# Optimization experiments

Measured on AMD Instinct MI355X. Metric: run time of the kernel, lower is better.

## Reference

```python
import jax, jax.numpy as jnp
import numpy as np
import math

D_MODEL = 1024
NUM_HEADS = 16


def setup_inputs() -> dict:
    key = jax.random.key(0)
    ks = jax.random.split(key, 5)
    B, S, D = 4, 2048, D_MODEL
    scale = 1.0 / math.sqrt(D)
    x = jax.random.normal(ks[0], (B, S, D), dtype=jnp.float32)
    wq = jax.random.normal(ks[1], (D, D), dtype=jnp.float32) * scale
    wk = jax.random.normal(ks[2], (D, D), dtype=jnp.float32) * scale
    wv = jax.random.normal(ks[3], (D, D), dtype=jnp.float32) * scale
    wo = jax.random.normal(ks[4], (D, D), dtype=jnp.float32) * scale
    return {"x": x, "wq": wq, "wk": wk, "wv": wv, "wo": wo}


def _mhsa(x, wq, wk, wv, wo):
    B, S, D = x.shape
    H = NUM_HEADS
    dk = D // H
    # projections: y = x @ W^T
    q = (x @ wq.T).reshape(B, S, H, dk).transpose(0, 2, 1, 3)  # [B,H,S,dk]
    k = (x @ wk.T).reshape(B, S, H, dk).transpose(0, 2, 1, 3)
    v = (x @ wv.T).reshape(B, S, H, dk).transpose(0, 2, 1, 3)
    scores = jnp.einsum("bhqd,bhkd->bhqk", q, k) / jnp.sqrt(jnp.asarray(dk, x.dtype))
    mask = jnp.tril(jnp.ones((S, S), dtype=bool))  # [S,S] causal
    neg_inf = jnp.asarray(-jnp.inf, scores.dtype)
    scores_masked = jnp.where(mask, scores, neg_inf)
    max_scores = jnp.max(scores_masked, axis=-1, keepdims=True)
    max_scores = jnp.where(jnp.isfinite(max_scores), max_scores, jnp.zeros_like(max_scores))
    exp_scores = jnp.exp(scores - max_scores) * mask.astype(scores.dtype)
    denom = jnp.maximum(exp_scores.sum(axis=-1, keepdims=True), 1e-9)
    attn = exp_scores / denom
    out = jnp.einsum("bhqk,bhkd->bhqd", attn, v)  # [B,H,S,dk]
    out = out.transpose(0, 2, 1, 3).reshape(B, S, D)
    return out @ wo.T


def reference(x, wq, wk, wv, wo):
    return _mhsa(x, wq, wk, wv, wo)
```

## Files before the change

### kernel.cpp

```cpp
#include <hip/hip_runtime.h>
#include <stdint.h>


typedef __attribute__((ext_vector_type(8))) short short8;
typedef __attribute__((ext_vector_type(4))) short short4v;
typedef __attribute__((ext_vector_type(4))) float float4v;
typedef __attribute__((ext_vector_type(2))) unsigned int uint2v;

#define QSCALE 0.18033688011112042f
#define EXP_C2 5.770780163555852f

__device__ inline short f2bf(float f) {
  union { float f; uint32_t u; } v; v.f = f;
  uint32_t r = (v.u + 0x7fffu + ((v.u >> 16) & 1)) >> 16;
  return (short)(uint16_t)r;
}

__device__ inline unsigned int pack2bf(float a, float b) {
  union { float f; unsigned int u; } ua, ub;
  ua.f = a; ub.f = b;
  return __builtin_amdgcn_perm(ub.u, ua.u, 0x07060302u);
}

__device__ inline void async_copy16(const void* g, void* l) {
  __builtin_amdgcn_global_load_lds(
      (const __attribute__((address_space(1))) void*)g,
      (__attribute__((address_space(3))) void*)l, 16, 0, 0);
}

__global__ __launch_bounds__(256) void cvtAll(
    const float* __restrict__ x, const float* __restrict__ wq,
    const float* __restrict__ wk, const float* __restrict__ wv,
    const float* __restrict__ wo,
    short* __restrict__ xb, short* __restrict__ wqb, short* __restrict__ wkb,
    short* __restrict__ wvb, short* __restrict__ wob) {
  const int b = blockIdx.x;
  const float* s; short* d; int base;
  if (b < 8192) { s = x; d = xb; base = b; }
  else {
    const int wi = (b - 8192) >> 10; base = (b - 8192) & 1023;
    s = (wi == 0) ? wq : (wi == 1) ? wk : (wi == 2) ? wv : wo;
    d = (wi == 0) ? wqb : (wi == 1) ? wkb : (wi == 2) ? wvb : wob;
  }
  const size_t i = (size_t)base * 256 + threadIdx.x;
  const float4v v = *(const float4v*)(s + 4 * i);
  short4v o;
  o[0] = f2bf(v[0]); o[1] = f2bf(v[1]);
  o[2] = f2bf(v[2]); o[3] = f2bf(v[3]);
  *(short4v*)(d + 4 * i) = o;
}

template <int MODE>
__global__ __launch_bounds__(256) void gemm_bt(
    const short* __restrict__ A,
    const short* __restrict__ W0, const short* __restrict__ W1,
    const short* __restrict__ W2,
    short* __restrict__ Yb0, short* __restrict__ Yb1, short* __restrict__ Yb2,
    float* __restrict__ Yf) {
  constexpr int Kd = 1024;
  __shared__ __align__(16) short As[128 * 32];
  __shared__ __align__(16) short Bs[128 * 32];

  const int t = threadIdx.x;
  const int w = t >> 6, l = t & 63, l15 = l & 15, quad = l >> 4;
  const int wm = w >> 1, wn = w & 1;
  const int m0 = blockIdx.y * 128, n0 = blockIdx.x * 128;

  const short* W = W0;
  short* Yb = Yb0;
  float sc = 1.0f;
  if (MODE == 0) {
    if (blockIdx.z == 0) sc = QSCALE;
    else if (blockIdx.z == 1) { W = W1; Yb = Yb1; }
    else { W = W2; Yb = Yb2; }
  }

  float4v acc[4][4];
#pragma unroll
  for (int i = 0; i < 4; i++)
#pragma unroll
    for (int j = 0; j < 4; j++) acc[i][j] = (float4v){0.f, 0.f, 0.f, 0.f};

  const int r4 = t >> 2, c48 = (t & 3) * 8;
  const short* Wbase = W + (n0 + r4) * Kd + c48;
  short* AsW = &As[w * 512];
  short* BsW = &Bs[w * 512];
  const int i0 = m0 + r4;
  const int i1 = m0 + 64 + r4;

  for (int k0 = 0; k0 < Kd; k0 += 32) {
    if (MODE == 0) {
      async_copy16(A + (size_t)i0 * Kd + k0 + c48, AsW);
      async_copy16(A + (size_t)i1 * Kd + k0 + c48, AsW + 2048);
    } else {
      const int k = k0 + c48, h = k >> 6, dd = k & 63;
      async_copy16(A + ((((size_t)(i0 >> 11) * 16 + h) * 2048 + (i0 & 2047)) * 64 + dd), AsW);
      async_copy16(A + ((((size_t)(i1 >> 11) * 16 + h) * 2048 + (i1 & 2047)) * 64 + dd), AsW + 2048);
    }
    async_copy16(Wbase + k0, BsW);
    async_copy16(Wbase + 64 * Kd + k0, BsW + 2048);
    __syncthreads();
    short8 af[4], bf[4];
#pragma unroll
    for (int mi = 0; mi < 4; mi++)
      af[mi] = *(const short8*)&As[(wm * 64 + mi * 16 + l15) * 32 + quad * 8];
#pragma unroll
    for (int ni = 0; ni < 4; ni++)
      bf[ni] = *(const short8*)&Bs[(wn * 64 + ni * 16 + l15) * 32 + quad * 8];
#pragma unroll
    for (int mi = 0; mi < 4; mi++)
#pragma unroll
      for (int ni = 0; ni < 4; ni++)
        acc[mi][ni] = __builtin_amdgcn_mfma_f32_16x16x32_bf16(
            af[mi], bf[ni], acc[mi][ni], 0, 0, 0);
    __syncthreads();
  }

#pragma unroll
  for (int mi = 0; mi < 4; mi++) {
    const int ib = m0 + wm * 64 + mi * 16 + quad * 4;
#pragma unroll
    for (int ni = 0; ni < 4; ni++) {
      const int j = n0 + wn * 64 + ni * 16 + l15;
#pragma unroll
      for (int r = 0; r < 4; r++) {
        const int i = ib + r;
        if (MODE == 0) {
          Yb[((((size_t)(i >> 11) * 16 + (j >> 6)) * 2048 + (i & 2047)) * 64 + (j & 63))] =
              f2bf(acc[mi][ni][r] * sc);
        } else {
          Yf[(size_t)i * 1024 + j] = acc[mi][ni][r];
        }
      }
    }
  }
}

__global__ __launch_bounds__(256) void transV(const short* __restrict__ V,
                                              short* __restrict__ VT) {
  __shared__ __align__(16) short Ls[64 * 72];
  const int t = threadIdx.x;
  const int s0 = blockIdx.x * 64, bh = blockIdx.y;
  const short* Vh = V + (size_t)bh * 2048 * 64;
  short* Th = VT + (size_t)bh * 64 * 2048;
  const int r = t >> 2, c = (t & 3) * 16;
  *(short8*)&Ls[r * 72 + c] = *(const short8*)&Vh[(size_t)(s0 + r) * 64 + c];
  *(short8*)&Ls[r * 72 + c + 8] = *(const short8*)&Vh[(size_t)(s0 + r) * 64 + c + 8];
  __syncthreads();
  short8 o0, o1;
#pragma unroll
  for (int j = 0; j < 8; j++) {
    o0[j] = Ls[(c + j) * 72 + r];
    o1[j] = Ls[(c + 8 + j) * 72 + r];
  }
  *(short8*)&Th[(size_t)r * 2048 + s0 + c] = o0;
  *(short8*)&Th[(size_t)r * 2048 + s0 + c + 8] = o1;
}

__global__ __launch_bounds__(256) void attn4(
    short* __restrict__ Q,
    const short* __restrict__ K,
    const short* __restrict__ VT) {
  __shared__ __align__(16) short Ks[2][64 * 64];
  __shared__ __align__(16) short Vs[2][64 * 64];
  __shared__ __align__(16) short Ps[4][16 * 64];

  const int t = threadIdx.x;
  const int w = t >> 6, l = t & 63, l15 = l & 15, quad = l >> 4;
  const int bh = blockIdx.x;
  const int qp = blockIdx.y;
  short* Qh = Q + (size_t)bh * 2048 * 64;
  const short* Kh = K + (size_t)bh * 2048 * 64;
  const short* Vh = VT + (size_t)bh * 64 * 2048;

  const int sr = t >> 2, c0 = t & 3;
  const int ssw = sr & 7;
  const int stA = sr * 64 + (((2 * c0) ^ ssw) << 3);
  const int stB = sr * 64 + (((2 * c0 + 1) ^ ssw) << 3);
  const int gA = c0 * 16, gB = c0 * 16 + 8;

  const int fsw = l15 & 7;
  const int fc0 = (quad ^ fsw) << 3;
  const int fc1 = ((4 + quad) ^ fsw) << 3;
  short* PsW = &Ps[w][0];
  const int pwr = l15 * 64;

  short8 ones;
#pragma unroll
  for (int j = 0; j < 8; j++) ones[j] = (short)0x3F80;
  const float4v initC = (float4v){-EXP_C2, -EXP_C2, -EXP_C2, -EXP_C2};

  for (int pass = 0; pass < 2; pass++) {
    const int q0 = (pass ? (31 - qp) : qp) * 64;
    const int qn = q0 + w * 16 + l15;
    const short8 qf0 = *(const short8*)&Qh[(size_t)qn * 64 + quad * 8];
    const short8 qf1 = *(const short8*)&Qh[(size_t)qn * 64 + 32 + quad * 8];

    float4v acc[4];
#pragma unroll
    for (int dt = 0; dt < 4; dt++) acc[dt] = (float4v){0.f, 0.f, 0.f, 0.f};
    float4v accL = (float4v){0.f, 0.f, 0.f, 0.f};

    short8 kv0 = *(const short8*)&Kh[(size_t)sr * 64 + gA];
    short8 kv1 = *(const short8*)&Kh[(size_t)sr * 64 + gB];
    short8 vv0 = *(const short8*)&Vh[(size_t)sr * 2048 + gA];
    short8 vv1 = *(const short8*)&Vh[(size_t)sr * 2048 + gB];

    int p = 0;
    for (int kb = 0; kb <= q0; kb += 64, p ^= 1) {
      const bool diag = (kb == q0);
      short* KsP = &Ks[p][0];
      short* VsP = &Vs[p][0];
      *(short8*)&KsP[stA] = kv0;
      *(short8*)&KsP[stB] = kv1;
      *(short8*)&VsP[stA] = vv0;
      *(short8*)&VsP[stB] = vv1;
      __syncthreads();

      const int kb2 = diag ? kb : kb + 64;
      kv0 = *(const short8*)&Kh[(size_t)(kb2 + sr) * 64 + gA];
      kv1 = *(const short8*)&Kh[(size_t)(kb2 + sr) * 64 + gB];
      vv0 = *(const short8*)&Vh[(size_t)sr * 2048 + kb2 + gA];
      vv1 = *(const short8*)&Vh[(size_t)sr * 2048 + kb2 + gB];

#pragma unroll
      for (int kt = 0; kt < 4; kt++) {
        const int krb = (kt * 16 + l15) * 64;
        const short8 kf0 = *(const short8*)&KsP[krb + fc0];
        const short8 kf1 = *(const short8*)&KsP[krb + fc1];
        float4v s = __builtin_amdgcn_mfma_f32_16x16x32_bf16(kf0, qf0, initC, 0, 0, 0);
        s = __builtin_amdgcn_mfma_f32_16x16x32_bf16(kf1, qf1, s, 0, 0, 0);
        float p0 = __builtin_amdgcn_exp2f(s[0]);
        float p1 = __builtin_amdgcn_exp2f(s[1]);
        float p2 = __builtin_amdgcn_exp2f(s[2]);
        float p3 = __builtin_amdgcn_exp2f(s[3]);
        if (diag) {
          const int key = kb + kt * 16 + quad * 4;
          p0 = (key <= qn) ? p0 : 0.f;
          p1 = (key + 1 <= qn) ? p1 : 0.f;
          p2 = (key + 2 <= qn) ? p2 : 0.f;
          p3 = (key + 3 <= qn) ? p3 : 0.f;
        }
        uint2v pw;
        pw[0] = pack2bf(p0, p1);
        pw[1] = pack2bf(p2, p3);
        *(uint2v*)&PsW[pwr + (((2 * kt + (quad >> 1)) ^ fsw) << 3) +
                       ((quad & 1) << 2)] = pw;
      }
      __builtin_amdgcn_wave_barrier();

      const short8 pf0 = *(const short8*)&PsW[pwr + fc0];
      const short8 pf1 = *(const short8*)&PsW[pwr + fc1];
#pragma unroll
      for (int dt = 0; dt < 4; dt++) {
        const int vrb = (dt * 16 + l15) * 64;
        const short8 vf0 = *(const short8*)&VsP[vrb + fc0];
        const short8 vf1 = *(const short8*)&VsP[vrb + fc1];
        acc[dt] = __builtin_amdgcn_mfma_f32_16x16x32_bf16(vf0, pf0, acc[dt], 0, 0, 0);
        acc[dt] = __builtin_amdgcn_mfma_f32_16x16x32_bf16(vf1, pf1, acc[dt], 0, 0, 0);
      }
      accL = __builtin_amdgcn_mfma_f32_16x16x32_bf16(ones, pf0, accL, 0, 0, 0);
      accL = __builtin_amdgcn_mfma_f32_16x16x32_bf16(ones, pf1, accL, 0, 0, 0);
    }

    const float inv = 1.0f / fmaxf(accL[0], 1e-30f);
#pragma unroll
    for (int dt = 0; dt < 4; dt++) {
      short4v o;
#pragma unroll
      for (int ri = 0; ri < 4; ri++) o[ri] = f2bf(acc[dt][ri] * inv);
      *(short4v*)&Qh[(size_t)qn * 64 + dt * 16 + quad * 4] = o;
    }
    if (pass == 0) __syncthreads();
  }
}

extern "C" void kernel_launch(void* const* d_in, const int* in_sizes, int n_in,
                              void* d_out, int out_size, void* d_ws,
                              size_t ws_size, hipStream_t stream) {
  const float* x = (const float*)d_in[0];
  const float* wq = (const float*)d_in[1];
  const float* wk = (const float*)d_in[2];
  const float* wv = (const float*)d_in[3];
  const float* wo = (const float*)d_in[4];
  float* out = (float*)d_out;

  short* xb = (short*)d_out;
  short* vtg = xb + (size_t)8192 * 1024;

  short* wqb = (short*)d_ws;
  short* wkb = wqb + (size_t)1024 * 1024;
  short* wvb = wkb + (size_t)1024 * 1024;
  short* wob = wvb + (size_t)1024 * 1024;
  short* qws = wob + (size_t)1024 * 1024;
  short* kws = qws + (size_t)8192 * 1024;
  short* vws = kws + (size_t)8192 * 1024;

  cvtAll<<<12288, 256, 0, stream>>>(x, wq, wk, wv, wo, xb, wqb, wkb, wvb, wob);
  gemm_bt<0><<<dim3(8, 64, 3), 256, 0, stream>>>(
      xb, wqb, wkb, wvb, qws, kws, vws, nullptr);
  transV<<<dim3(32, 64), 256, 0, stream>>>(vws, vtg);
  attn4<<<dim3(64, 16), 256, 0, stream>>>(qws, kws, vtg);
  gemm_bt<1><<<dim3(8, 64, 1), 256, 0, stream>>>(
      qws, wob, nullptr, nullptr, nullptr, nullptr, nullptr, out);
}
```

Before: 259.1 us.

## Fuse V transpose into QKV GEMM epilogue and remap blocks for XCD locality

```diff
diff --git a/kernel.cpp b/kernel.cpp
--- a/kernel.cpp
+++ b/kernel.cpp
@@ -64,14 +64,24 @@
   const int t = threadIdx.x;
   const int w = t >> 6, l = t & 63, l15 = l & 15, quad = l >> 4;
   const int wm = w >> 1, wn = w & 1;
-  const int m0 = blockIdx.y * 128, n0 = blockIdx.x * 128;
+
+  int mblk, nblk, zz = 0;
+  {
+    const int o = blockIdx.x;
+    const int xcd = o & 7, slot = o >> 3;
+    mblk = (xcd << 3) | (slot & 7);
+    const int c = slot >> 3;
+    if (MODE == 0) { nblk = c & 7; zz = c >> 3; }
+    else nblk = c;
+  }
+  const int m0 = mblk * 128, n0 = nblk * 128;
 
   const short* W = W0;
   short* Yb = Yb0;
   float sc = 1.0f;
   if (MODE == 0) {
-    if (blockIdx.z == 0) sc = QSCALE;
-    else if (blockIdx.z == 1) { W = W1; Yb = Yb1; }
+    if (zz == 0) sc = QSCALE;
+    else if (zz == 1) { W = W1; Yb = Yb1; }
     else { W = W2; Yb = Yb2; }
   }
 
@@ -122,39 +132,26 @@
 #pragma unroll
     for (int ni = 0; ni < 4; ni++) {
       const int j = n0 + wn * 64 + ni * 16 + l15;
-#pragma unroll
-      for (int r = 0; r < 4; r++) {
-        const int i = ib + r;
-        if (MODE == 0) {
-          Yb[((((size_t)(i >> 11) * 16 + (j >> 6)) * 2048 + (i & 2047)) * 64 + (j & 63))] =
-              f2bf(acc[mi][ni][r] * sc);
-        } else {
-          Yf[(size_t)i * 1024 + j] = acc[mi][ni][r];
+      if (MODE == 0 && zz == 2) {
+        short4v o;
+#pragma unroll
+        for (int r = 0; r < 4; r++) o[r] = f2bf(acc[mi][ni][r]);
+        *(short4v*)&Yb[(((size_t)(ib >> 11) * 16 + (j >> 6)) * 64 + (j & 63)) * 2048 +
+                       (ib & 2047)] = o;
+      } else {
+#pragma unroll
+        for (int r = 0; r < 4; r++) {
+          const int i = ib + r;
+          if (MODE == 0) {
+            Yb[((((size_t)(i >> 11) * 16 + (j >> 6)) * 2048 + (i & 2047)) * 64 + (j & 63))] =
+                f2bf(acc[mi][ni][r] * sc);
+          } else {
+            Yf[(size_t)i * 1024 + j] = acc[mi][ni][r];
+          }
         }
       }
     }
   }
-}
-
-__global__ __launch_bounds__(256) void transV(const short* __restrict__ V,
-                                              short* __restrict__ VT) {
-  __shared__ __align__(16) short Ls[64 * 72];
-  const int t = threadIdx.x;
-  const int s0 = blockIdx.x * 64, bh = blockIdx.y;
-  const short* Vh = V + (size_t)bh * 2048 * 64;
-  short* Th = VT + (size_t)bh * 64 * 2048;
-  const int r = t >> 2, c = (t & 3) * 16;
-  *(short8*)&Ls[r * 72 + c] = *(const short8*)&Vh[(size_t)(s0 + r) * 64 + c];
-  *(short8*)&Ls[r * 72 + c + 8] = *(const short8*)&Vh[(size_t)(s0 + r) * 64 + c + 8];
-  __syncthreads();
-  short8 o0, o1;
-#pragma unroll
-  for (int j = 0; j < 8; j++) {
-    o0[j] = Ls[(c + j) * 72 + r];
-    o1[j] = Ls[(c + 8 + j) * 72 + r];
-  }
-  *(short8*)&Th[(size_t)r * 2048 + s0 + c] = o0;
-  *(short8*)&Th[(size_t)r * 2048 + s0 + c + 8] = o1;
 }
 
 __global__ __launch_bounds__(256) void attn4(
@@ -294,13 +291,11 @@
   short* wob = wvb + (size_t)1024 * 1024;
   short* qws = wob + (size_t)1024 * 1024;
   short* kws = qws + (size_t)8192 * 1024;
-  short* vws = kws + (size_t)8192 * 1024;
 
   cvtAll<<<12288, 256, 0, stream>>>(x, wq, wk, wv, wo, xb, wqb, wkb, wvb, wob);
-  gemm_bt<0><<<dim3(8, 64, 3), 256, 0, stream>>>(
-      xb, wqb, wkb, wvb, qws, kws, vws, nullptr);
-  transV<<<dim3(32, 64), 256, 0, stream>>>(vws, vtg);
+  gemm_bt<0><<<1536, 256, 0, stream>>>(
+      xb, wqb, wkb, wvb, qws, kws, vtg, nullptr);
   attn4<<<dim3(64, 16), 256, 0, stream>>>(qws, kws, vtg);
-  gemm_bt<1><<<dim3(8, 64, 1), 256, 0, stream>>>(
+  gemm_bt<1><<<512, 256, 0, stream>>>(
       qws, wob, nullptr, nullptr, nullptr, nullptr, nullptr, out);
 }
```

After: 253.4 us. 1.02x faster.
